# Optimization experiments

Measured on AMD Instinct MI355X. Metric: run time of the kernel, lower is better.

## Reference

```python
import jax, jax.numpy as jnp
import numpy as np
from jax import lax

B = 32768
IMG = 28
K = 3
OUT_HW = IMG - K + 1  # 26
FLAT = OUT_HW * OUT_HW  # 676
HID = 300
NCLS = 10


def setup_inputs() -> dict:
    key = jax.random.key(0)
    ks = jax.random.split(key, 8)
    x = jax.random.normal(ks[0], (B, IMG * IMG), dtype=jnp.float32)
    conv_w = jax.random.normal(ks[1], (K, K), dtype=jnp.float32) * 0.1
    # Linear params stored as (in, out) so forward is h @ W + b
    W1 = jax.random.normal(ks[2], (FLAT, HID), dtype=jnp.float32) * 0.04
    b1 = jnp.zeros((HID,), dtype=jnp.float32)
    W2 = jax.random.normal(ks[3], (HID, HID), dtype=jnp.float32) * 0.06
    b2 = jnp.zeros((HID,), dtype=jnp.float32)
    W3 = jax.random.normal(ks[4], (HID, NCLS), dtype=jnp.float32) * 0.06
    b3 = jnp.zeros((NCLS,), dtype=jnp.float32)
    return {"x": x, "conv_w": conv_w, "W1": W1, "b1": b1,
            "W2": W2, "b2": b2, "W3": W3, "b3": b3}


def reference(x, conv_w, W1, b1, W2, b2, W3, b3):
    b = x.shape[0]
    img = x.reshape(b, 1, IMG, IMG)  # NCHW
    # Valid cross-correlation with 3x3 kernel -> [B,1,26,26]
    y = lax.conv_general_dilated(
        img, conv_w[None, None, :, :], window_strides=(1, 1), padding="VALID",
        dimension_numbers=("NCHW", "OIHW", "NCHW"))
    h = y.reshape(b, FLAT)
    h = jax.nn.relu(h @ W1 + b1)
    h = jax.nn.relu(h @ W2 + b2)
    return h @ W3 + b3
```

## Files before the change

kernel.cpp:

```cpp
#include <hip/hip_runtime.h>


typedef __bf16 bf16_t;
typedef __bf16 bf16x8 __attribute__((ext_vector_type(8)));
typedef float  f32x4  __attribute__((ext_vector_type(4)));

#define MFMA16(a, b, c) __builtin_amdgcn_mfma_f32_16x16x32_bf16((a), (b), (c), 0, 0, 0)

#define W1F_ELEMS (25 * 20 * 64 * 8)
#define W2F_ELEMS (10 * 20 * 64 * 8)
#define W3F_ELEMS (10 * 1 * 64 * 8)

__global__ void prep_weights(const float* __restrict__ conv_w,
                             const float* __restrict__ W1,
                             const float* __restrict__ W2,
                             const float* __restrict__ W3,
                             bf16_t* __restrict__ W1f,
                             bf16_t* __restrict__ W2f,
                             bf16_t* __restrict__ W3f) {
    int idx = blockIdx.x * 256 + threadIdx.x;
    if (idx < 800 * 320) {
        int k = idx / 320;
        int n = idx - k * 320;
        float v = 0.0f;
        if (k < 784 && n < 300) {
            int py = k / 28;
            int px = k - py * 28;
#pragma unroll
            for (int ky = 0; ky < 3; ++ky) {
                int oy = py - ky;
                if (oy < 0 || oy > 25) continue;
#pragma unroll
                for (int kx = 0; kx < 3; ++kx) {
                    int ox = px - kx;
                    if (ox < 0 || ox > 25) continue;
                    v += conv_w[ky * 3 + kx] * W1[(oy * 26 + ox) * 300 + n];
                }
            }
        }
        int kc = k >> 5, quad = (k >> 3) & 3, j = k & 7;
        int nt = n >> 4, nin = n & 15;
        W1f[(((kc * 20 + nt) * 64 + quad * 16 + nin) << 3) + j] = (bf16_t)v;
    } else if (idx < 800 * 320 + 320 * 320) {
        int i2 = idx - 800 * 320;
        int k = i2 / 320;
        int n = i2 - k * 320;
        float v = (k < 300 && n < 300) ? W2[k * 300 + n] : 0.0f;
        int kc = k >> 5, quad = (k >> 3) & 3, j = k & 7;
        int nt = n >> 4, nin = n & 15;
        W2f[(((kc * 20 + nt) * 64 + quad * 16 + nin) << 3) + j] = (bf16_t)v;
    } else if (idx < 800 * 320 + 320 * 320 + 320 * 16) {
        int i3 = idx - (800 * 320 + 320 * 320);
        int k = i3 / 16;
        int n = i3 - k * 16;
        float v = (k < 300 && n < 10) ? W3[k * 10 + n] : 0.0f;
        int kc = k >> 5, quad = (k >> 3) & 3, j = k & 7;
        W3f[(((kc * 64) + quad * 16 + n) << 3) + j] = (bf16_t)v;
    }
}

__device__ __forceinline__ void stage16(const bf16x8* g, bf16x8* l) {
    __builtin_amdgcn_global_load_lds(
        (const __attribute__((address_space(1))) void*)g,
        (__attribute__((address_space(3))) void*)l, 16, 0, 0);
}

__global__ __launch_bounds__(512, 4) void fused_mlp(
    const float* __restrict__ x, const float* __restrict__ b1,
    const float* __restrict__ b2, const float* __restrict__ b3,
    const bf16x8* __restrict__ W1f, const bf16x8* __restrict__ W2f,
    const bf16x8* __restrict__ W3f, float* __restrict__ out) {
    __shared__ bf16x8 arena[3840];
    bf16x8* bufB1 = arena;
    bf16x8* hbuf  = arena;
    bf16x8* bufB2 = arena + 2560;

    const int tid = threadIdx.x;
    const int w   = tid >> 6;
    const int l   = tid & 63;
    const int mh  = w & 1;
    const int nq  = w >> 1;
    const int q   = l >> 4;
    const int l15 = l & 15;
    const int r0  = blockIdx.x * 64;

    const float* rowA = x + (size_t)(r0 + mh * 32 + l15) * 784;
    const float* rowB = rowA + 16 * 784;

    float bias1[5], bias2[5];
#pragma unroll
    for (int nt = 0; nt < 5; ++nt) {
        int n = (nq * 5 + nt) * 16 + l15;
        bias1[nt] = (n < 300) ? b1[n] : 0.0f;
        bias2[nt] = (n < 300) ? b2[n] : 0.0f;
    }
    float bias3 = (w < 4 && l15 < 10) ? b3[l15] : 0.0f;

    for (int t = w; t < 20; t += 8) stage16(W1f + (t * 64 + l), bufB1 + t * 64);
    for (int t = w; t < 20; t += 8) stage16(W2f + (t * 64 + l), bufB2 + t * 64);

    float4 ua0, ua1, ub0, ub1;
    {
        const float4* pa = (const float4*)(rowA + q * 8);
        const float4* pb = (const float4*)(rowB + q * 8);
        ua0 = pa[0]; ua1 = pa[1]; ub0 = pb[0]; ub1 = pb[1];
    }

    f32x4 acc[2][5];
#pragma unroll
    for (int m = 0; m < 2; ++m)
#pragma unroll
        for (int nt = 0; nt < 5; ++nt) acc[m][nt] = (f32x4){0.f, 0.f, 0.f, 0.f};

    for (int kc = 0; kc < 25; ++kc) {
        __syncthreads();

        if (kc + 1 < 25) {
            int s1 = (kc + 1) & 1;
            for (int t = w; t < 20; t += 8)
                stage16(W1f + (((kc + 1) * 20 + t) * 64 + l),
                        bufB1 + s1 * 1280 + t * 64);
        }

        bf16x8 afA, afB;
        afA[0] = (bf16_t)ua0.x; afA[1] = (bf16_t)ua0.y;
        afA[2] = (bf16_t)ua0.z; afA[3] = (bf16_t)ua0.w;
        afA[4] = (bf16_t)ua1.x; afA[5] = (bf16_t)ua1.y;
        afA[6] = (bf16_t)ua1.z; afA[7] = (bf16_t)ua1.w;
        afB[0] = (bf16_t)ub0.x; afB[1] = (bf16_t)ub0.y;
        afB[2] = (bf16_t)ub0.z; afB[3] = (bf16_t)ub0.w;
        afB[4] = (bf16_t)ub1.x; afB[5] = (bf16_t)ub1.y;
        afB[6] = (bf16_t)ub1.z; afB[7] = (bf16_t)ub1.w;

        if (kc + 1 < 25) {
            int k0 = (kc + 1) * 32 + q * 8;
            if (k0 < 784) {
                const float4* pa = (const float4*)(rowA + k0);
                const float4* pb = (const float4*)(rowB + k0);
                ua0 = pa[0]; ua1 = pa[1]; ub0 = pb[0]; ub1 = pb[1];
            } else {
                ua0 = ua1 = ub0 = ub1 = make_float4(0.f, 0.f, 0.f, 0.f);
            }
        }

        const bf16x8* bb = bufB1 + (kc & 1) * 1280 + (nq * 5) * 64 + l;
#pragma unroll
        for (int nt = 0; nt < 5; ++nt) {
            bf16x8 b = bb[nt * 64];
            acc[0][nt] = MFMA16(afA, b, acc[0][nt]);
            acc[1][nt] = MFMA16(afB, b, acc[1][nt]);
        }
    }
    __syncthreads();

    {
        bf16_t* hb = (bf16_t*)hbuf;
#pragma unroll
        for (int nt = 0; nt < 5; ++nt) {
            int n = (nq * 5 + nt) * 16 + l15;
            int kc2 = n >> 5, quad = (n >> 3) & 3, j = n & 7;
#pragma unroll
            for (int mt2 = 0; mt2 < 2; ++mt2) {
                int mt = mh * 2 + mt2;
#pragma unroll
                for (int r = 0; r < 4; ++r) {
                    float v = acc[mt2][nt][r] + bias1[nt];
                    v = v > 0.f ? v : 0.f;
                    hb[(((kc2 * 4 + mt) * 64 + quad * 16 + q * 4 + r) << 3) + j] =
                        (bf16_t)v;
                }
            }
        }
    }
    __syncthreads();

#pragma unroll
    for (int m = 0; m < 2; ++m)
#pragma unroll
        for (int nt = 0; nt < 5; ++nt) acc[m][nt] = (f32x4){0.f, 0.f, 0.f, 0.f};
    for (int kc = 0; kc < 10; ++kc) {
        bf16x8 a0 = hbuf[(kc * 4 + mh * 2 + 0) * 64 + l];
        bf16x8 a1 = hbuf[(kc * 4 + mh * 2 + 1) * 64 + l];
        const bf16x8* bb = bufB2 + (nq * 5) * 64 + l;
#pragma unroll
        for (int nt = 0; nt < 5; ++nt) {
            bf16x8 b = bb[nt * 64];
            acc[0][nt] = MFMA16(a0, b, acc[0][nt]);
            acc[1][nt] = MFMA16(a1, b, acc[1][nt]);
        }
        if (kc + 1 < 10) {
            __syncthreads();
            for (int t = w; t < 20; t += 8)
                stage16(W2f + (((kc + 1) * 20 + t) * 64 + l), bufB2 + t * 64);
            __syncthreads();
        }
    }
    __syncthreads();

    {
        bf16_t* hb = (bf16_t*)hbuf;
#pragma unroll
        for (int nt = 0; nt < 5; ++nt) {
            int n = (nq * 5 + nt) * 16 + l15;
            int kc2 = n >> 5, quad = (n >> 3) & 3, j = n & 7;
#pragma unroll
            for (int mt2 = 0; mt2 < 2; ++mt2) {
                int mt = mh * 2 + mt2;
#pragma unroll
                for (int r = 0; r < 4; ++r) {
                    float v = acc[mt2][nt][r] + bias2[nt];
                    v = v > 0.f ? v : 0.f;
                    hb[(((kc2 * 4 + mt) * 64 + quad * 16 + q * 4 + r) << 3) + j] =
                        (bf16_t)v;
                }
            }
        }
    }
    __syncthreads();

    for (int t = w; t < 10; t += 8) stage16(W3f + (t * 64 + l), bufB2 + t * 64);
    __syncthreads();

    if (w < 4) {
        f32x4 acc3 = (f32x4){0.f, 0.f, 0.f, 0.f};
        for (int kc = 0; kc < 10; ++kc)
            acc3 = MFMA16(hbuf[(kc * 4 + w) * 64 + l], bufB2[kc * 64 + l], acc3);
        if (l15 < 10) {
#pragma unroll
            for (int r = 0; r < 4; ++r)
                out[(size_t)(r0 + w * 16 + q * 4 + r) * 10 + l15] = acc3[r] + bias3;
        }
    }
}

extern "C" void kernel_launch(void* const* d_in, const int* in_sizes, int n_in,
                              void* d_out, int out_size, void* d_ws, size_t ws_size,
                              hipStream_t stream) {
    const float* x      = (const float*)d_in[0];
    const float* conv_w = (const float*)d_in[1];
    const float* W1     = (const float*)d_in[2];
    const float* b1     = (const float*)d_in[3];
    const float* W2     = (const float*)d_in[4];
    const float* b2     = (const float*)d_in[5];
    const float* W3     = (const float*)d_in[6];
    const float* b3     = (const float*)d_in[7];
    float* out = (float*)d_out;

    char* ws = (char*)d_ws;
    bf16_t* W1f = (bf16_t*)(ws);
    bf16_t* W2f = (bf16_t*)(ws + (size_t)W1F_ELEMS * 2);
    bf16_t* W3f = (bf16_t*)(ws + (size_t)(W1F_ELEMS + W2F_ELEMS) * 2);
    if (ws_size < (size_t)(W1F_ELEMS + W2F_ELEMS + W3F_ELEMS) * 2) return;

    int prep_total = 800 * 320 + 320 * 320 + 320 * 16;
    prep_weights<<<(prep_total + 255) / 256, 256, 0, stream>>>(
        conv_w, W1, W2, W3, W1f, W2f, W3f);

    fused_mlp<<<32768 / 64, 512, 0, stream>>>(
        x, b1, b2, b3, (const bf16x8*)W1f, (const bf16x8*)W2f,
        (const bf16x8*)W3f, out);
}
```

Before: 202.2 us.

## Split fused MLP into two kernels with bf16 hidden activations in global memory

Splits the single fused kernel into gemm1 (conv-folded GEMM1 plus bias and ReLU, writing bf16 h1 to workspace) and gemm23 (GEMM2 and GEMM3). Each kernel then needs less shared memory, and GEMM2 now double-buffers its W2 tiles with prefetch instead of the serialized stage/sync pattern. W3 is read directly from global memory. The cost is an extra round trip of about 21 MB of h1 through global memory and one more kernel launch.

```diff
diff --git a/kernel.cpp b/kernel.cpp
--- a/kernel.cpp
+++ b/kernel.cpp
@@ -10,6 +10,8 @@
 #define W1F_ELEMS (25 * 20 * 64 * 8)
 #define W2F_ELEMS (10 * 20 * 64 * 8)
 #define W3F_ELEMS (10 * 1 * 64 * 8)
+#define H1_OFF    768000
+#define H1_BYTES  ((size_t)32768 * 320 * 2)
 
 __global__ void prep_weights(const float* __restrict__ conv_w,
                              const float* __restrict__ W1,
@@ -65,15 +67,10 @@
         (__attribute__((address_space(3))) void*)l, 16, 0, 0);
 }
 
-__global__ __launch_bounds__(512, 4) void fused_mlp(
+__global__ __launch_bounds__(512, 4) void gemm1(
     const float* __restrict__ x, const float* __restrict__ b1,
-    const float* __restrict__ b2, const float* __restrict__ b3,
-    const bf16x8* __restrict__ W1f, const bf16x8* __restrict__ W2f,
-    const bf16x8* __restrict__ W3f, float* __restrict__ out) {
-    __shared__ bf16x8 arena[3840];
-    bf16x8* bufB1 = arena;
-    bf16x8* hbuf  = arena;
-    bf16x8* bufB2 = arena + 2560;
+    const bf16x8* __restrict__ W1f, bf16_t* __restrict__ h1) {
+    __shared__ bf16x8 bufB[2 * 1280];
 
     const int tid = threadIdx.x;
     const int w   = tid >> 6;
@@ -87,18 +84,7 @@
     const float* rowA = x + (size_t)(r0 + mh * 32 + l15) * 784;
     const float* rowB = rowA + 16 * 784;
 
-    float bias1[5], bias2[5];
-#pragma unroll
-    for (int nt = 0; nt < 5; ++nt) {
-        int n = (nq * 5 + nt) * 16 + l15;
-        bias1[nt] = (n < 300) ? b1[n] : 0.0f;
-        bias2[nt] = (n < 300) ? b2[n] : 0.0f;
-    }
-    float bias3 = (w < 4 && l15 < 10) ? b3[l15] : 0.0f;
-
-    for (int t = w; t < 20; t += 8) stage16(W1f + (t * 64 + l), bufB1 + t * 64);
-    for (int t = w; t < 20; t += 8) stage16(W2f + (t * 64 + l), bufB2 + t * 64);
-
+    for (int t = w; t < 20; t += 8) stage16(W1f + (t * 64 + l), bufB + t * 64);
     float4 ua0, ua1, ub0, ub1;
     {
         const float4* pa = (const float4*)(rowA + q * 8);
@@ -119,7 +105,7 @@
             int s1 = (kc + 1) & 1;
             for (int t = w; t < 20; t += 8)
                 stage16(W1f + (((kc + 1) * 20 + t) * 64 + l),
-                        bufB1 + s1 * 1280 + t * 64);
+                        bufB + s1 * 1280 + t * 64);
         }
 
         bf16x8 afA, afB;
@@ -143,7 +129,7 @@
             }
         }
 
-        const bf16x8* bb = bufB1 + (kc & 1) * 1280 + (nq * 5) * 64 + l;
+        const bf16x8* bb = bufB + (kc & 1) * 1280 + (nq * 5) * 64 + l;
 #pragma unroll
         for (int nt = 0; nt < 5; ++nt) {
             bf16x8 b = bb[nt * 64];
@@ -151,20 +137,91 @@
             acc[1][nt] = MFMA16(afB, b, acc[1][nt]);
         }
     }
+
+#pragma unroll
+    for (int nt = 0; nt < 5; ++nt) {
+        int n = (nq * 5 + nt) * 16 + l15;
+        float bias = (n < 300) ? b1[n] : 0.0f;
+#pragma unroll
+        for (int mt2 = 0; mt2 < 2; ++mt2) {
+            int mt = mh * 2 + mt2;
+#pragma unroll
+            for (int r = 0; r < 4; ++r) {
+                float v = acc[mt2][nt][r] + bias;
+                v = v > 0.f ? v : 0.f;
+                h1[(size_t)(r0 + mt * 16 + q * 4 + r) * 320 + n] = (bf16_t)v;
+            }
+        }
+    }
+}
+
+__global__ __launch_bounds__(512, 4) void gemm23(
+    const bf16_t* __restrict__ h1, const float* __restrict__ b2,
+    const float* __restrict__ b3, const bf16x8* __restrict__ W2f,
+    const bf16x8* __restrict__ W3f, float* __restrict__ out) {
+    __shared__ bf16x8 arena[2560];
+
+    const int tid = threadIdx.x;
+    const int w   = tid >> 6;
+    const int l   = tid & 63;
+    const int mh  = w & 1;
+    const int nq  = w >> 1;
+    const int q   = l >> 4;
+    const int l15 = l & 15;
+    const int r0  = blockIdx.x * 64;
+
+    const bf16_t* rowA = h1 + (size_t)(r0 + mh * 32 + l15) * 320;
+    const bf16_t* rowB = rowA + 16 * 320;
+
+    for (int t = w; t < 20; t += 8) stage16(W2f + (t * 64 + l), arena + t * 64);
+    bf16x8 uaA = *(const bf16x8*)(rowA + q * 8);
+    bf16x8 uaB = *(const bf16x8*)(rowB + q * 8);
+
+    f32x4 acc[2][5];
+#pragma unroll
+    for (int m = 0; m < 2; ++m)
+#pragma unroll
+        for (int nt = 0; nt < 5; ++nt) acc[m][nt] = (f32x4){0.f, 0.f, 0.f, 0.f};
+
+    for (int kc = 0; kc < 10; ++kc) {
+        __syncthreads();
+
+        if (kc + 1 < 10) {
+            int s1 = (kc + 1) & 1;
+            for (int t = w; t < 20; t += 8)
+                stage16(W2f + (((kc + 1) * 20 + t) * 64 + l),
+                        arena + s1 * 1280 + t * 64);
+        }
+
+        bf16x8 afA = uaA, afB = uaB;
+        if (kc + 1 < 10) {
+            uaA = *(const bf16x8*)(rowA + (kc + 1) * 32 + q * 8);
+            uaB = *(const bf16x8*)(rowB + (kc + 1) * 32 + q * 8);
+        }
+
+        const bf16x8* bb = arena + (kc & 1) * 1280 + (nq * 5) * 64 + l;
+#pragma unroll
+        for (int nt = 0; nt < 5; ++nt) {
+            bf16x8 b = bb[nt * 64];
+            acc[0][nt] = MFMA16(afA, b, acc[0][nt]);
+            acc[1][nt] = MFMA16(afB, b, acc[1][nt]);
+        }
+    }
     __syncthreads();
 
     {
-        bf16_t* hb = (bf16_t*)hbuf;
+        bf16_t* hb = (bf16_t*)arena;
 #pragma unroll
         for (int nt = 0; nt < 5; ++nt) {
             int n = (nq * 5 + nt) * 16 + l15;
+            float bias = (n < 300) ? b2[n] : 0.0f;
             int kc2 = n >> 5, quad = (n >> 3) & 3, j = n & 7;
 #pragma unroll
             for (int mt2 = 0; mt2 < 2; ++mt2) {
                 int mt = mh * 2 + mt2;
 #pragma unroll
                 for (int r = 0; r < 4; ++r) {
-                    float v = acc[mt2][nt][r] + bias1[nt];
+                    float v = acc[mt2][nt][r] + bias;
                     v = v > 0.f ? v : 0.f;
                     hb[(((kc2 * 4 + mt) * 64 + quad * 16 + q * 4 + r) << 3) + j] =
                         (bf16_t)v;
@@ -174,61 +231,18 @@
     }
     __syncthreads();
 
-#pragma unroll
-    for (int m = 0; m < 2; ++m)
-#pragma unroll
-        for (int nt = 0; nt < 5; ++nt) acc[m][nt] = (f32x4){0.f, 0.f, 0.f, 0.f};
-    for (int kc = 0; kc < 10; ++kc) {
-        bf16x8 a0 = hbuf[(kc * 4 + mh * 2 + 0) * 64 + l];
-        bf16x8 a1 = hbuf[(kc * 4 + mh * 2 + 1) * 64 + l];
-        const bf16x8* bb = bufB2 + (nq * 5) * 64 + l;
-#pragma unroll
-        for (int nt = 0; nt < 5; ++nt) {
-            bf16x8 b = bb[nt * 64];
-            acc[0][nt] = MFMA16(a0, b, acc[0][nt]);
-            acc[1][nt] = MFMA16(a1, b, acc[1][nt]);
-        }
-        if (kc + 1 < 10) {
-            __syncthreads();
-            for (int t = w; t < 20; t += 8)
-                stage16(W2f + (((kc + 1) * 20 + t) * 64 + l), bufB2 + t * 64);
-            __syncthreads();
-        }
-    }
-    __syncthreads();
-
-    {
-        bf16_t* hb = (bf16_t*)hbuf;
-#pragma unroll
-        for (int nt = 0; nt < 5; ++nt) {
-            int n = (nq * 5 + nt) * 16 + l15;
-            int kc2 = n >> 5, quad = (n >> 3) & 3, j = n & 7;
-#pragma unroll
-            for (int mt2 = 0; mt2 < 2; ++mt2) {
-                int mt = mh * 2 + mt2;
-#pragma unroll
-                for (int r = 0; r < 4; ++r) {
-                    float v = acc[mt2][nt][r] + bias2[nt];
-                    v = v > 0.f ? v : 0.f;
-                    hb[(((kc2 * 4 + mt) * 64 + quad * 16 + q * 4 + r) << 3) + j] =
-                        (bf16_t)v;
-                }
-            }
-        }
-    }
-    __syncthreads();
-
-    for (int t = w; t < 10; t += 8) stage16(W3f + (t * 64 + l), bufB2 + t * 64);
-    __syncthreads();
-
     if (w < 4) {
         f32x4 acc3 = (f32x4){0.f, 0.f, 0.f, 0.f};
-        for (int kc = 0; kc < 10; ++kc)
-            acc3 = MFMA16(hbuf[(kc * 4 + w) * 64 + l], bufB2[kc * 64 + l], acc3);
+        for (int kc = 0; kc < 10; ++kc) {
+            bf16x8 a = arena[(kc * 4 + w) * 64 + l];
+            bf16x8 b = W3f[kc * 64 + l];
+            acc3 = MFMA16(a, b, acc3);
+        }
         if (l15 < 10) {
+            float bias = b3[l15];
 #pragma unroll
             for (int r = 0; r < 4; ++r)
-                out[(size_t)(r0 + w * 16 + q * 4 + r) * 10 + l15] = acc3[r] + bias3;
+                out[(size_t)(r0 + w * 16 + q * 4 + r) * 10 + l15] = acc3[r] + bias;
         }
     }
 }
@@ -250,13 +264,15 @@
     bf16_t* W1f = (bf16_t*)(ws);
     bf16_t* W2f = (bf16_t*)(ws + (size_t)W1F_ELEMS * 2);
     bf16_t* W3f = (bf16_t*)(ws + (size_t)(W1F_ELEMS + W2F_ELEMS) * 2);
-    if (ws_size < (size_t)(W1F_ELEMS + W2F_ELEMS + W3F_ELEMS) * 2) return;
+    bf16_t* h1  = (bf16_t*)(ws + H1_OFF);
+    if (ws_size < H1_OFF + H1_BYTES) return;
 
     int prep_total = 800 * 320 + 320 * 320 + 320 * 16;
     prep_weights<<<(prep_total + 255) / 256, 256, 0, stream>>>(
         conv_w, W1, W2, W3, W1f, W2f, W3f);
 
-    fused_mlp<<<32768 / 64, 512, 0, stream>>>(
-        x, b1, b2, b3, (const bf16x8*)W1f, (const bf16x8*)W2f,
-        (const bf16x8*)W3f, out);
-}
+    gemm1<<<32768 / 64, 512, 0, stream>>>(x, b1, (const bf16x8*)W1f, h1);
+
+    gemm23<<<32768 / 64, 512, 0, stream>>>(
+        h1, b2, b3, (const bf16x8*)W2f, (const bf16x8*)W3f, out);
+}
```

New measurement: 215.8 us. +6.7%, slower.
